# Kernel optimization log

Measured on AMD Instinct MI355X. Metric: run time of the kernel, lower is better.

## Reference

```python
import math
import jax, jax.numpy as jnp
import numpy as np

B, T, D = 8, 2048, 512
EPS = 1e-5


def _gate(x, W, b, a, g, beta):
    # Linear -> PReLU (single shared slope a) -> LayerNorm -> sigmoid
    h = x @ W.T + b
    h = jnp.where(h >= 0, h, a * h)
    mu = jnp.mean(h, axis=-1, keepdims=True)
    var = jnp.var(h, axis=-1, keepdims=True)
    h = (h - mu) / jnp.sqrt(var + EPS) * g + beta
    return jax.nn.sigmoid(h)


def setup_inputs() -> dict:
    key = jax.random.key(0)
    ks = jax.random.split(key, 12)
    lin = lambda k: jax.random.normal(k, (D, D), jnp.float32) * 0.02
    z = jnp.zeros((D,), jnp.float32)
    o = jnp.ones((D,), jnp.float32)
    a0 = jnp.float32(0.25)  # PReLU default init
    inp = {
        "query": jax.random.normal(ks[0], (B, T, D), jnp.float32),
        "value": jax.random.normal(ks[1], (B, T, D), jnp.float32),
        "aux_emb": jax.random.normal(ks[2], (B, 1, D), jnp.float32),
        # ragged valid lengths in [T//2, T] to keep every sample realistic
        "input_len": jax.random.randint(ks[3], (B,), T // 2, T + 1),
        "Wq": lin(ks[4]), "bq": z,
        "Wqg": lin(ks[5]), "bqg": z, "aq": a0, "gq": o, "betaq": z,
        "Wkg": lin(ks[6]), "bkg": z, "ak": a0, "gk": o, "betak": z,
        "Wvg": lin(ks[7]), "bvg": z, "av": a0, "gv": o, "betav": z,
        "Wsig": lin(ks[8]), "bsig": z,
        "Wtan": lin(ks[9]), "btan": z,
    }
    return inp


def reference(query, value, aux_emb, input_len,
              Wq, bq,
              Wqg, bqg, aq, gq, betaq,
              Wkg, bkg, ak, gk, betak,
              Wvg, bvg, av, gv, betav,
              Wsig, bsig, Wtan, btan):
    q = query @ Wq.T + bq
    q = q * _gate(aux_emb, Wqg, bqg, aq, gq, betaq)          # [B,T,D]
    k = value * _gate(aux_emb, Wkg, bkg, ak, gk, betak)      # [B,T,D]
    vg = _gate(aux_emb, Wvg, bvg, av, gv, betav)             # [B,1,D]
    vg = jax.nn.sigmoid(vg @ Wsig.T + bsig) * jnp.tanh(vg @ Wtan.T + btan)
    v = value * vg                                           # [B,T,D]

    w = jnp.einsum('btd,bsd->bts', q, k) / math.sqrt(D)      # [B,T,T]
    r = jnp.arange(T)
    causal = (r[:, None] >= r[None, :]).astype(w.dtype)      # tril ones
    w = w * causal
    w = jnp.where(w == 0.0, -jnp.inf, w)  # torch quirk: exact zeros -> -inf
    L = input_len[:, None, None]                              # [B,1,1]
    invalid = (r[None, :, None] < L) & (r[None, None, :] >= L)
    w = jnp.where(invalid, -jnp.inf, w)
    p = jax.nn.softmax(w, axis=-1)
    # rows beyond input_len are padding: zero them (torch code produced NaN
    # there via -inf*0; intended semantics is zeroed padding rows)
    row_valid = (r[None, :, None] < L).astype(p.dtype)        # [B,T,1]
    p = p * row_valid
    return p @ v                                              # [B,T,D]
```

## Files before the change

### kernel.cpp

```cpp
#include <hip/hip_runtime.h>
#include <hip/hip_bf16.h>
#include <stdint.h>

#define BB 8
#define TT 2048
#define DD 512

typedef __attribute__((ext_vector_type(8))) __bf16 bf16x8;
typedef __attribute__((ext_vector_type(4))) float f32x4;

__device__ __forceinline__ unsigned short f2bf(float f) {
    unsigned u = __builtin_bit_cast(unsigned, f);
    unsigned r = u + 0x7fffu + ((u >> 16) & 1u);
    return (unsigned short)(r >> 16);
}

__device__ __forceinline__ void gload_lds16(const unsigned short* g, unsigned short* l) {
    __builtin_amdgcn_global_load_lds(
        (const __attribute__((address_space(1))) void*)g,
        (__attribute__((address_space(3))) void*)l, 16, 0, 0);
}

__global__ __launch_bounds__(256) void gates_mv1(
    const float* __restrict__ aux,
    const float* __restrict__ Wqg, const float* __restrict__ bqg, const float* __restrict__ aq,
    const float* __restrict__ Wkg, const float* __restrict__ bkg, const float* __restrict__ ak,
    const float* __restrict__ Wvg, const float* __restrict__ bvg, const float* __restrict__ av,
    float* __restrict__ h) {
    __shared__ float saux[BB * DD];
    int tid = threadIdx.x;
#pragma unroll
    for (int i = 0; i < 4; i++) {
        int idx = tid + i * 256;
        ((float4*)saux)[idx] = ((const float4*)aux)[idx];
    }
    __syncthreads();
    int wave = (blockIdx.x * 256 + tid) >> 6;
    int lane = tid & 63;
    int g = wave >> 9, r = wave & 511;
    const float* W    = (g == 0) ? Wqg : (g == 1) ? Wkg : Wvg;
    const float* bias = (g == 0) ? bqg : (g == 1) ? bkg : bvg;
    const float* alpha = (g == 0) ? aq : (g == 1) ? ak : av;
    const float4* Wrow = (const float4*)(W + (size_t)r * DD);
    float acc[BB];
#pragma unroll
    for (int b = 0; b < BB; b++) acc[b] = 0.f;
#pragma unroll
    for (int c = 0; c < 2; c++) {
        float4 w4 = Wrow[lane + c * 64];
#pragma unroll
        for (int b = 0; b < BB; b++) {
            float4 a4 = ((const float4*)(saux + b * DD))[lane + c * 64];
            acc[b] += w4.x * a4.x + w4.y * a4.y + w4.z * a4.z + w4.w * a4.w;
        }
    }
#pragma unroll
    for (int b = 0; b < BB; b++) {
#pragma unroll
        for (int s = 1; s < 64; s <<= 1) acc[b] += __shfl_xor(acc[b], s, 64);
    }
    if (lane == 0) {
        float bi = bias[r], a = alpha[0];
#pragma unroll
        for (int b = 0; b < BB; b++) {
            float v = acc[b] + bi;
            v = (v >= 0.f) ? v : a * v;
            h[(g * BB + b) * DD + r] = v;
        }
    }
}

__global__ __launch_bounds__(512) void gates_norm(
    const float* __restrict__ h,
    const float* __restrict__ gq, const float* __restrict__ betaq,
    const float* __restrict__ gk, const float* __restrict__ betak,
    const float* __restrict__ gv, const float* __restrict__ betav,
    float* __restrict__ qgate, float* __restrict__ kgate, float* __restrict__ vg) {
    int g = blockIdx.x >> 3, b = blockIdx.x & 7, tid = threadIdx.x;
    __shared__ float red[DD], red2[DD];
    float hv = h[(g * BB + b) * DD + tid];
    red[tid] = hv; red2[tid] = hv * hv;
    __syncthreads();
    for (int s = 256; s > 0; s >>= 1) {
        if (tid < s) { red[tid] += red[tid + s]; red2[tid] += red2[tid + s]; }
        __syncthreads();
    }
    float mu = red[0] * (1.f / DD);
    float var = red2[0] * (1.f / DD) - mu * mu;
    const float* gg = (g == 0) ? gq : (g == 1) ? gk : gv;
    const float* be = (g == 0) ? betaq : (g == 1) ? betak : betav;
    float val = (hv - mu) * rsqrtf(var + 1e-5f) * gg[tid] + be[tid];
    float sg = 1.f / (1.f + expf(-val));
    float* outp = (g == 0) ? qgate : (g == 1) ? kgate : vg;
    outp[b * DD + tid] = sg;
}

__global__ __launch_bounds__(256) void gates_mv2(
    const float* __restrict__ vg,
    const float* __restrict__ Wsig, const float* __restrict__ bsig,
    const float* __restrict__ Wtan, const float* __restrict__ btan,
    float* __restrict__ vgate) {
    __shared__ float svg[BB * DD];
    int tid = threadIdx.x;
#pragma unroll
    for (int i = 0; i < 4; i++) {
        int idx = tid + i * 256;
        ((float4*)svg)[idx] = ((const float4*)vg)[idx];
    }
    __syncthreads();
    int r = (blockIdx.x * 256 + tid) >> 6;
    int lane = tid & 63;
    const float4* Ws = (const float4*)(Wsig + (size_t)r * DD);
    const float4* Wt = (const float4*)(Wtan + (size_t)r * DD);
    float as_[BB], at_[BB];
#pragma unroll
    for (int b = 0; b < BB; b++) { as_[b] = 0.f; at_[b] = 0.f; }
#pragma unroll
    for (int c = 0; c < 2; c++) {
        float4 w1 = Ws[lane + c * 64];
        float4 w2 = Wt[lane + c * 64];
#pragma unroll
        for (int b = 0; b < BB; b++) {
            float4 a4 = ((const float4*)(svg + b * DD))[lane + c * 64];
            as_[b] += w1.x * a4.x + w1.y * a4.y + w1.z * a4.z + w1.w * a4.w;
            at_[b] += w2.x * a4.x + w2.y * a4.y + w2.z * a4.z + w2.w * a4.w;
        }
    }
#pragma unroll
    for (int b = 0; b < BB; b++) {
#pragma unroll
        for (int s = 1; s < 64; s <<= 1) {
            as_[b] += __shfl_xor(as_[b], s, 64);
            at_[b] += __shfl_xor(at_[b], s, 64);
        }
    }
    if (lane == 0) {
        float b1 = bsig[r], b2 = btan[r];
#pragma unroll
        for (int b = 0; b < BB; b++) {
            float s1 = 1.f / (1.f + expf(-(as_[b] + b1)));
            float s2 = tanhf(at_[b] + b2);
            vgate[b * DD + r] = s1 * s2;
        }
    }
}

__global__ __launch_bounds__(256) void prep_kernel(
    const float* __restrict__ query, unsigned short* __restrict__ queryb) {
    int idx = blockIdx.x * 256 + threadIdx.x;
    float4 q4 = ((const float4*)query)[idx];
    ushort4 oq;
    oq.x = f2bf(q4.x); oq.y = f2bf(q4.y); oq.z = f2bf(q4.z); oq.w = f2bf(q4.w);
    ((ushort4*)queryb)[idx] = oq;
}

__global__ __launch_bounds__(256) void wconv_kernel(const float* __restrict__ Wq,
                                                    unsigned short* __restrict__ Wqb) {
    int idx = blockIdx.x * 256 + threadIdx.x;
    float4 w4 = ((const float4*)Wq)[idx];
    ushort4 o;
    o.x = f2bf(w4.x); o.y = f2bf(w4.y); o.z = f2bf(w4.z); o.w = f2bf(w4.w);
    ((ushort4*)Wqb)[idx] = o;
}

__global__ __launch_bounds__(256) void vk_kernel(const float* __restrict__ value,
                                                 const float* __restrict__ kgate,
                                                 const float* __restrict__ vgate,
                                                 unsigned short* __restrict__ kb,
                                                 unsigned short* __restrict__ vbT) {
    __shared__ float tile[32][33];
    int b = blockIdx.z;
    int t0 = blockIdx.x * 32, d0 = blockIdx.y * 32;
    int tx = threadIdx.x, ty = threadIdx.y;
    float kg = kgate[b * DD + d0 + tx];
#pragma unroll
    for (int i = 0; i < 4; i++) {
        int t = t0 + ty + i * 8;
        float v = value[((size_t)b * TT + t) * DD + d0 + tx];
        tile[ty + i * 8][tx] = v;
        kb[((size_t)b * TT + t) * DD + d0 + tx] = f2bf(v * kg);
    }
    __syncthreads();
#pragma unroll
    for (int i = 0; i < 4; i++) {
        int d = d0 + ty + i * 8;
        float g = vgate[b * DD + d];
        vbT[((size_t)b * DD + d) * TT + t0 + tx] = f2bf(tile[tx][ty + i * 8] * g);
    }
}

#define GEMM_CORE(APTR, ALDA, BPTR, BLDA, KSTART, KEND)                                   \
    __shared__ __align__(16) unsigned short As[128 * 32];                                 \
    __shared__ __align__(16) unsigned short Bs[128 * 32];                                 \
    int tid = threadIdx.x;                                                                \
    int lane = tid & 63, wid = tid >> 6;                                                  \
    int wm = (wid >> 1) * 64, wn = (wid & 1) * 64;                                        \
    int lm = lane & 15, quad = lane >> 4;                                                 \
    f32x4 acc[4][4];                                                                      \
    _Pragma("unroll") for (int im = 0; im < 4; im++)                                      \
        _Pragma("unroll") for (int in = 0; in < 4; in++)                                  \
            acc[im][in] = (f32x4){0.f, 0.f, 0.f, 0.f};                                    \
    for (int k0 = (KSTART); k0 < (KEND); k0 += 32) {                                      \
        _Pragma("unroll") for (int i = 0; i < 2; i++) {                                   \
            int idx = tid * 8 + i * 2048;                                                 \
            int r = idx >> 5;                                                             \
            int cg = ((idx >> 3) & 3) ^ ((r >> 1) & 3);                                   \
            gload_lds16(&(APTR)[(size_t)r * (ALDA) + k0 + cg * 8], &As[idx]);             \
            gload_lds16(&(BPTR)[(size_t)r * (BLDA) + k0 + cg * 8], &Bs[idx]);             \
        }                                                                                 \
        __syncthreads();                                                                  \
        bf16x8 af[4], bf_[4];                                                             \
        _Pragma("unroll") for (int i = 0; i < 4; i++) {                                   \
            int row = wm + i * 16 + lm;                                                   \
            af[i] = *(const bf16x8*)&As[row * 32 + (quad ^ ((row >> 1) & 3)) * 8];        \
        }                                                                                 \
        _Pragma("unroll") for (int i = 0; i < 4; i++) {                                   \
            int row = wn + i * 16 + lm;                                                   \
            bf_[i] = *(const bf16x8*)&Bs[row * 32 + (quad ^ ((row >> 1) & 3)) * 8];       \
        }                                                                                 \
        _Pragma("unroll") for (int im = 0; im < 4; im++)                                  \
            _Pragma("unroll") for (int in = 0; in < 4; in++)                              \
                acc[im][in] = __builtin_amdgcn_mfma_f32_16x16x32_bf16(af[im], bf_[in],    \
                                                                     acc[im][in], 0, 0, 0);\
        __syncthreads();                                                                  \
    }

__global__ __launch_bounds__(256) void qgemm_kernel(
    const unsigned short* __restrict__ Amat, const unsigned short* __restrict__ Bmat,
    const float* __restrict__ bq, const float* __restrict__ qgate,
    unsigned short* __restrict__ qb) {
    int m0 = blockIdx.x * 128, n0 = blockIdx.y * 128;
    const unsigned short* Ap = Amat + (size_t)m0 * DD;
    const unsigned short* Bp = Bmat + (size_t)n0 * DD;
    GEMM_CORE(Ap, DD, Bp, DD, 0, DD)
    int b = m0 >> 11;
#pragma unroll
    for (int im = 0; im < 4; im++) {
        int row = m0 + wm + im * 16 + quad * 4;
#pragma unroll
        for (int in = 0; in < 4; in++) {
            int col = n0 + wn + in * 16 + lm;
            float bias = bq[col];
            float g = qgate[b * DD + col];
#pragma unroll
            for (int r = 0; r < 4; r++) {
                float v = (acc[im][in][r] + bias) * g;
                qb[(size_t)(row + r) * DD + col] = f2bf(v);
            }
        }
    }
}

__global__ __launch_bounds__(256) void scores_kernel(
    const unsigned short* __restrict__ qb, const unsigned short* __restrict__ kb,
    unsigned short* __restrict__ P, float* __restrict__ rowsum) {
    int b = blockIdx.z;
    int idx = blockIdx.x;
    int mt = (int)((sqrtf(8.f * idx + 1.f) - 1.f) * 0.5f);
    while ((mt + 1) * (mt + 2) / 2 <= idx) mt++;
    while (mt * (mt + 1) / 2 > idx) mt--;
    int nt = idx - mt * (mt + 1) / 2;
    int t0 = mt * 128, s0 = nt * 128;
    const unsigned short* Ap = qb + ((size_t)b * TT + t0) * DD;
    const unsigned short* Bp = kb + ((size_t)b * TT + s0) * DD;
    GEMM_CORE(Ap, DD, Bp, DD, 0, DD)
    const float scale = 0.044194173824159216f;
    unsigned short* Pb = P + (size_t)b * TT * TT;
#pragma unroll
    for (int im = 0; im < 4; im++) {
        int tbase = t0 + wm + im * 16 + quad * 4;
        float rs[4] = {0.f, 0.f, 0.f, 0.f};
#pragma unroll
        for (int in = 0; in < 4; in++) {
            int s = s0 + wn + in * 16 + lm;
#pragma unroll
            for (int r = 0; r < 4; r++) {
                float p = (s <= tbase + r) ? expf(acc[im][in][r] * scale) : 0.f;
                Pb[(size_t)(tbase + r) * TT + s] = f2bf(p);
                rs[r] += p;
            }
        }
#pragma unroll
        for (int r = 0; r < 4; r++) {
            float v = rs[r];
            v += __shfl_xor(v, 1, 64);
            v += __shfl_xor(v, 2, 64);
            v += __shfl_xor(v, 4, 64);
            v += __shfl_xor(v, 8, 64);
            if (lm == 0) atomicAdd(&rowsum[b * TT + tbase + r], v);
        }
    }
}

__global__ __launch_bounds__(256) void out_kernel(
    const unsigned short* __restrict__ P, const unsigned short* __restrict__ vbT,
    const float* __restrict__ rowsum, const int* __restrict__ input_len,
    float* __restrict__ out) {
    int nt = blockIdx.x, mt = blockIdx.y, b = blockIdx.z;
    int t0 = mt * 128, n0 = nt * 128;
    const unsigned short* Ap = P + (size_t)b * TT * TT + (size_t)t0 * TT;
    const unsigned short* Bp = vbT + ((size_t)b * DD + n0) * TT;
    int kend = (mt + 1) * 128;
    GEMM_CORE(Ap, TT, Bp, TT, 0, kend)
    int L = input_len[b];
#pragma unroll
    for (int im = 0; im < 4; im++) {
        int tbase = t0 + wm + im * 16 + quad * 4;
#pragma unroll
        for (int r = 0; r < 4; r++) {
            int t = tbase + r;
            float denom = rowsum[b * TT + t];
            float inv = 1.f / denom;
            bool valid = (t < L);
#pragma unroll
            for (int in = 0; in < 4; in++) {
                int n = n0 + wn + in * 16 + lm;
                float o = valid ? acc[im][in][r] * inv : 0.f;
                out[((size_t)b * TT + t) * DD + n] = o;
            }
        }
    }
}

extern "C" void kernel_launch(void* const* d_in, const int* in_sizes, int n_in,
                              void* d_out, int out_size, void* d_ws, size_t ws_size,
                              hipStream_t stream) {
    const float* query = (const float*)d_in[0];
    const float* value = (const float*)d_in[1];
    const float* aux   = (const float*)d_in[2];
    const int*   ilen  = (const int*)d_in[3];
    const float* Wq    = (const float*)d_in[4];
    const float* bq    = (const float*)d_in[5];
    const float* Wqg   = (const float*)d_in[6];
    const float* bqg   = (const float*)d_in[7];
    const float* aq    = (const float*)d_in[8];
    const float* gq    = (const float*)d_in[9];
    const float* betaq = (const float*)d_in[10];
    const float* Wkg   = (const float*)d_in[11];
    const float* bkg   = (const float*)d_in[12];
    const float* ak    = (const float*)d_in[13];
    const float* gk    = (const float*)d_in[14];
    const float* betak = (const float*)d_in[15];
    const float* Wvg   = (const float*)d_in[16];
    const float* bvg   = (const float*)d_in[17];
    const float* av    = (const float*)d_in[18];
    const float* gv    = (const float*)d_in[19];
    const float* betav = (const float*)d_in[20];
    const float* Wsig  = (const float*)d_in[21];
    const float* bsig  = (const float*)d_in[22];
    const float* Wtan  = (const float*)d_in[23];
    const float* btan  = (const float*)d_in[24];

    char* ws = (char*)d_ws;
    float* qgate          = (float*)(ws + 0);
    float* kgate          = (float*)(ws + 16384);
    float* vgate          = (float*)(ws + 32768);
    float* rowsum         = (float*)(ws + 49152);
    unsigned short* Wqb   = (unsigned short*)(ws + 114688);
    unsigned short* queryb= (unsigned short*)(ws + 638976);
    unsigned short* qb    = (unsigned short*)(ws + 17416192);
    unsigned short* kb    = (unsigned short*)(ws + 34193408);
    unsigned short* vbT   = (unsigned short*)(ws + 50970624);
    unsigned short* P     = (unsigned short*)(ws + 67747840);
    float* hbuf           = (float*)(ws + 67747840);
    float* vg             = (float*)(ws + 67747840 + 49152);

    hipMemsetAsync(rowsum, 0, BB * TT * sizeof(float), stream);

    gates_mv1<<<384, 256, 0, stream>>>(aux, Wqg, bqg, aq, Wkg, bkg, ak, Wvg, bvg, av, hbuf);
    gates_norm<<<24, 512, 0, stream>>>(hbuf, gq, betaq, gk, betak, gv, betav,
                                       qgate, kgate, vg);
    gates_mv2<<<128, 256, 0, stream>>>(vg, Wsig, bsig, Wtan, btan, vgate);

    prep_kernel<<<(BB * TT * DD / 4) / 256, 256, 0, stream>>>(query, queryb);
    wconv_kernel<<<(DD * DD / 4) / 256, 256, 0, stream>>>(Wq, Wqb);
    vk_kernel<<<dim3(TT / 32, DD / 32, BB), dim3(32, 8), 0, stream>>>(value, kgate, vgate, kb, vbT);
    qgemm_kernel<<<dim3((BB * TT) / 128, DD / 128), 256, 0, stream>>>(queryb, Wqb, bq, qgate, qb);
    scores_kernel<<<dim3(136, 1, BB), 256, 0, stream>>>(qb, kb, P, rowsum);
    out_kernel<<<dim3(DD / 128, TT / 128, BB), 256, 0, stream>>>(P, vbT, rowsum, ilen, (float*)d_out);
}
```

Before: 294.5 us.

## Pack causal P tiles contiguously, split out GEMM rows, and merge convert kernels

Scores now write each lower-triangular 128x128 P tile into a packed tile array instead of a dense TxT matrix. The output GEMM reads those packed tiles, uses 64-row M tiles with heaviest rows scheduled first to balance causal work, and doubles the grid. The three conversion kernels are merged into one launch. The goals are less P memory footprint and better locality, better load balance, and fewer launches, at the cost of more re-reads of vbT from the smaller M tiles.

```diff
diff --git a/kernel.cpp b/kernel.cpp
--- a/kernel.cpp
+++ b/kernel.cpp
@@ -145,47 +145,46 @@
     }
 }
 
-__global__ __launch_bounds__(256) void prep_kernel(
-    const float* __restrict__ query, unsigned short* __restrict__ queryb) {
-    int idx = blockIdx.x * 256 + threadIdx.x;
-    float4 q4 = ((const float4*)query)[idx];
-    ushort4 oq;
-    oq.x = f2bf(q4.x); oq.y = f2bf(q4.y); oq.z = f2bf(q4.z); oq.w = f2bf(q4.w);
-    ((ushort4*)queryb)[idx] = oq;
-}
-
-__global__ __launch_bounds__(256) void wconv_kernel(const float* __restrict__ Wq,
-                                                    unsigned short* __restrict__ Wqb) {
-    int idx = blockIdx.x * 256 + threadIdx.x;
-    float4 w4 = ((const float4*)Wq)[idx];
-    ushort4 o;
-    o.x = f2bf(w4.x); o.y = f2bf(w4.y); o.z = f2bf(w4.z); o.w = f2bf(w4.w);
-    ((ushort4*)Wqb)[idx] = o;
-}
-
-__global__ __launch_bounds__(256) void vk_kernel(const float* __restrict__ value,
-                                                 const float* __restrict__ kgate,
-                                                 const float* __restrict__ vgate,
-                                                 unsigned short* __restrict__ kb,
-                                                 unsigned short* __restrict__ vbT) {
+__global__ __launch_bounds__(256) void convert_kernel(
+    const float* __restrict__ query, const float* __restrict__ Wq,
+    const float* __restrict__ value,
+    const float* __restrict__ kgate, const float* __restrict__ vgate,
+    unsigned short* __restrict__ queryb, unsigned short* __restrict__ Wqb,
+    unsigned short* __restrict__ kb, unsigned short* __restrict__ vbT) {
     __shared__ float tile[32][33];
-    int b = blockIdx.z;
-    int t0 = blockIdx.x * 32, d0 = blockIdx.y * 32;
-    int tx = threadIdx.x, ty = threadIdx.y;
-    float kg = kgate[b * DD + d0 + tx];
-#pragma unroll
-    for (int i = 0; i < 4; i++) {
-        int t = t0 + ty + i * 8;
-        float v = value[((size_t)b * TT + t) * DD + d0 + tx];
-        tile[ty + i * 8][tx] = v;
-        kb[((size_t)b * TT + t) * DD + d0 + tx] = f2bf(v * kg);
-    }
-    __syncthreads();
-#pragma unroll
-    for (int i = 0; i < 4; i++) {
-        int d = d0 + ty + i * 8;
-        float g = vgate[b * DD + d];
-        vbT[((size_t)b * DD + d) * TT + t0 + tx] = f2bf(tile[tx][ty + i * 8] * g);
+    int bi = blockIdx.x, tid = threadIdx.x;
+    if (bi < 8192) {
+        int idx = bi * 256 + tid;
+        float4 q4 = ((const float4*)query)[idx];
+        ushort4 oq;
+        oq.x = f2bf(q4.x); oq.y = f2bf(q4.y); oq.z = f2bf(q4.z); oq.w = f2bf(q4.w);
+        ((ushort4*)queryb)[idx] = oq;
+    } else if (bi < 8448) {
+        int idx = (bi - 8192) * 256 + tid;
+        float4 w4 = ((const float4*)Wq)[idx];
+        ushort4 o;
+        o.x = f2bf(w4.x); o.y = f2bf(w4.y); o.z = f2bf(w4.z); o.w = f2bf(w4.w);
+        ((ushort4*)Wqb)[idx] = o;
+    } else {
+        int vb = bi - 8448;
+        int tIdx = vb & 63, dIdx = (vb >> 6) & 15, b = vb >> 10;
+        int t0 = tIdx * 32, d0 = dIdx * 32;
+        int tx = tid & 31, ty = tid >> 5;
+        float kg = kgate[b * DD + d0 + tx];
+#pragma unroll
+        for (int i = 0; i < 4; i++) {
+            int t = t0 + ty + i * 8;
+            float v = value[((size_t)b * TT + t) * DD + d0 + tx];
+            tile[ty + i * 8][tx] = v;
+            kb[((size_t)b * TT + t) * DD + d0 + tx] = f2bf(v * kg);
+        }
+        __syncthreads();
+#pragma unroll
+        for (int i = 0; i < 4; i++) {
+            int d = d0 + ty + i * 8;
+            float g = vgate[b * DD + d];
+            vbT[((size_t)b * DD + d) * TT + t0 + tx] = f2bf(tile[tx][ty + i * 8] * g);
+        }
     }
 }
 
@@ -265,18 +264,19 @@
     const unsigned short* Bp = kb + ((size_t)b * TT + s0) * DD;
     GEMM_CORE(Ap, DD, Bp, DD, 0, DD)
     const float scale = 0.044194173824159216f;
-    unsigned short* Pb = P + (size_t)b * TT * TT;
+    unsigned short* Ptile = P + ((size_t)b * 136 + (size_t)mt * (mt + 1) / 2 + nt) * 16384;
 #pragma unroll
     for (int im = 0; im < 4; im++) {
-        int tbase = t0 + wm + im * 16 + quad * 4;
+        int ltb = wm + im * 16 + quad * 4;
         float rs[4] = {0.f, 0.f, 0.f, 0.f};
 #pragma unroll
         for (int in = 0; in < 4; in++) {
-            int s = s0 + wn + in * 16 + lm;
+            int ls = wn + in * 16 + lm;
+            int s = s0 + ls;
 #pragma unroll
             for (int r = 0; r < 4; r++) {
-                float p = (s <= tbase + r) ? expf(acc[im][in][r] * scale) : 0.f;
-                Pb[(size_t)(tbase + r) * TT + s] = f2bf(p);
+                float p = (s <= t0 + ltb + r) ? expf(acc[im][in][r] * scale) : 0.f;
+                Ptile[(size_t)(ltb + r) * 128 + ls] = f2bf(p);
                 rs[r] += p;
             }
         }
@@ -287,7 +287,7 @@
             v += __shfl_xor(v, 2, 64);
             v += __shfl_xor(v, 4, 64);
             v += __shfl_xor(v, 8, 64);
-            if (lm == 0) atomicAdd(&rowsum[b * TT + tbase + r], v);
+            if (lm == 0) atomicAdd(&rowsum[b * TT + t0 + ltb + r], v);
         }
     }
 }
@@ -296,21 +296,72 @@
     const unsigned short* __restrict__ P, const unsigned short* __restrict__ vbT,
     const float* __restrict__ rowsum, const int* __restrict__ input_len,
     float* __restrict__ out) {
-    int nt = blockIdx.x, mt = blockIdx.y, b = blockIdx.z;
-    int t0 = mt * 128, n0 = nt * 128;
-    const unsigned short* Ap = P + (size_t)b * TT * TT + (size_t)t0 * TT;
-    const unsigned short* Bp = vbT + ((size_t)b * DD + n0) * TT;
+    int nt = blockIdx.x;
+    int mt2 = 31 - (int)blockIdx.y;
+    int b = blockIdx.z;
+    int t0 = mt2 * 64, n0 = nt * 128;
+    int mt = mt2 >> 1;
+    int rowoff = (mt2 & 1) * 64;
+    size_t triBase = ((size_t)b * 136 + (size_t)mt * (mt + 1) / 2) * 16384;
     int kend = (mt + 1) * 128;
-    GEMM_CORE(Ap, TT, Bp, TT, 0, kend)
+
+    __shared__ __align__(16) unsigned short As[64 * 32];
+    __shared__ __align__(16) unsigned short Bs[128 * 32];
+    int tid = threadIdx.x;
+    int lane = tid & 63, wid = tid >> 6;
+    int wm = (wid >> 1) * 32, wn = (wid & 1) * 64;
+    int lm = lane & 15, quad = lane >> 4;
+    f32x4 acc[2][4];
+#pragma unroll
+    for (int im = 0; im < 2; im++)
+#pragma unroll
+        for (int in = 0; in < 4; in++) acc[im][in] = (f32x4){0.f, 0.f, 0.f, 0.f};
+
+    for (int k0 = 0; k0 < kend; k0 += 32) {
+        {
+            int idx = tid * 8;
+            int r = idx >> 5;
+            int cg = ((idx >> 3) & 3) ^ ((r >> 1) & 3);
+            const unsigned short* ag = P + triBase + (size_t)(k0 >> 7) * 16384 +
+                                       (size_t)(rowoff + r) * 128 + (k0 & 127) + cg * 8;
+            gload_lds16(ag, &As[idx]);
+        }
+#pragma unroll
+        for (int i = 0; i < 2; i++) {
+            int idx = tid * 8 + i * 2048;
+            int r = idx >> 5;
+            int cg = ((idx >> 3) & 3) ^ ((r >> 1) & 3);
+            gload_lds16(&vbT[(size_t)(b * DD + n0 + r) * TT + k0 + cg * 8], &Bs[idx]);
+        }
+        __syncthreads();
+        bf16x8 af[2], bf_[4];
+#pragma unroll
+        for (int i = 0; i < 2; i++) {
+            int row = wm + i * 16 + lm;
+            af[i] = *(const bf16x8*)&As[row * 32 + (quad ^ ((row >> 1) & 3)) * 8];
+        }
+#pragma unroll
+        for (int i = 0; i < 4; i++) {
+            int row = wn + i * 16 + lm;
+            bf_[i] = *(const bf16x8*)&Bs[row * 32 + (quad ^ ((row >> 1) & 3)) * 8];
+        }
+#pragma unroll
+        for (int im = 0; im < 2; im++)
+#pragma unroll
+            for (int in = 0; in < 4; in++)
+                acc[im][in] = __builtin_amdgcn_mfma_f32_16x16x32_bf16(af[im], bf_[in],
+                                                                     acc[im][in], 0, 0, 0);
+        __syncthreads();
+    }
+
     int L = input_len[b];
 #pragma unroll
-    for (int im = 0; im < 4; im++) {
+    for (int im = 0; im < 2; im++) {
         int tbase = t0 + wm + im * 16 + quad * 4;
 #pragma unroll
         for (int r = 0; r < 4; r++) {
             int t = tbase + r;
-            float denom = rowsum[b * TT + t];
-            float inv = 1.f / denom;
+            float inv = 1.f / rowsum[b * TT + t];
             bool valid = (t < L);
 #pragma unroll
             for (int in = 0; in < 4; in++) {
@@ -372,10 +423,9 @@
                                        qgate, kgate, vg);
     gates_mv2<<<128, 256, 0, stream>>>(vg, Wsig, bsig, Wtan, btan, vgate);
 
-    prep_kernel<<<(BB * TT * DD / 4) / 256, 256, 0, stream>>>(query, queryb);
-    wconv_kernel<<<(DD * DD / 4) / 256, 256, 0, stream>>>(Wq, Wqb);
-    vk_kernel<<<dim3(TT / 32, DD / 32, BB), dim3(32, 8), 0, stream>>>(value, kgate, vgate, kb, vbT);
+    convert_kernel<<<16640, 256, 0, stream>>>(query, Wq, value, kgate, vgate,
+                                              queryb, Wqb, kb, vbT);
     qgemm_kernel<<<dim3((BB * TT) / 128, DD / 128), 256, 0, stream>>>(queryb, Wqb, bq, qgate, qb);
     scores_kernel<<<dim3(136, 1, BB), 256, 0, stream>>>(qb, kb, P, rowsum);
-    out_kernel<<<dim3(DD / 128, TT / 128, BB), 256, 0, stream>>>(P, vbT, rowsum, ilen, (float*)d_out);
-}
+    out_kernel<<<dim3(4, 32, BB), 256, 0, stream>>>(P, vbT, rowsum, ilen, (float*)d_out);
+}
```

Measured after the change: 297.4 us. No clear change (+1.0%).
